# Performance work log

Hardware: AMD Instinct MI355X
Metric: run time of the kernel (lower is better)

The kernel has to match this reference:

```python
import jax, jax.numpy as jnp
import numpy as np

M_BITS = 8   # mantissa bits (m in BlockQuantize)
E_BITS = 8   # exponent bits (e)
GROUP_D = 64 # column-group width from group_shapes [64,64]


def bfp_quantize_2d(W, d=GROUP_D, m=M_BITS, e=E_BITS):
    """Faithful vectorized BlockQuantize2D with calculate_bias=True.
    Groups = 64-wide column blocks spanning all rows (tensor.reshape(-1,d)[start::new_width])."""
    a, b = W.shape
    nw = b // d
    # [nw, a*d]: each row is one quantization group
    blocks = W.reshape(a, nw, d).transpose(1, 0, 2).reshape(nw, a * d)
    maxv = jnp.max(jnp.abs(blocks), axis=1, keepdims=True)
    bias = 2.0 ** e - jnp.log2(maxv) + jnp.log2(2.0 - 2.0 ** (-m + 1)) - 1.0
    max_exp = 2.0 ** e - 1.0 - bias
    max_val = 2.0 ** max_exp * (1.0 + (1.0 - 2.0 ** (-m - 1)))
    sign = jnp.sign(blocks)
    absx = jnp.clip(jnp.abs(blocks), -max_val, max_val)  # lower bound negative -> no-op, as in source
    exponent = jnp.floor(jnp.log2(absx + 1e-40))
    mantissa = absx / 2.0 ** exponent                    # in [1, 2)
    group_exp = jnp.max(exponent, axis=1, keepdims=True)
    group_exp = jnp.where(group_exp + bias < 1.0, -bias, group_exp)
    # shiftTruncateInBinaryForm
    factor = 2 ** (m - 1)                                # 128
    sm = (mantissa * factor).astype(jnp.int32)           # [128, 256)
    shift = jnp.clip((group_exp - exponent).astype(jnp.int32), 0, 31)
    shifted = jnp.right_shift(sm, shift)
    safe = jnp.maximum(shifted, 1)
    bitlen = (jnp.floor(jnp.log2(safe.astype(jnp.float32))) + 1.0).astype(jnp.int32)
    mask = jnp.where(bitlen > 8, jnp.left_shift(jnp.int32(255), bitlen - 8), jnp.int32(255))
    trunc = jnp.bitwise_and(shifted, mask).astype(jnp.float32) / factor
    q = sign * trunc * 2.0 ** group_exp
    return q.reshape(nw, a, d).transpose(1, 0, 2).reshape(a, b)


def apply_rope(t, cos, sin):
    """t: [b,s,h,hd]; complex rotation on (even, odd) pairs as in apply_rotary_emb."""
    tr = t.reshape(*t.shape[:-1], -1, 2)
    te, to = tr[..., 0], tr[..., 1]
    c = cos[None, :, None, :]
    s = sin[None, :, None, :]
    oe = te * c - to * s
    oo = te * s + to * c
    return jnp.stack([oe, oo], axis=-1).reshape(t.shape)


def setup_inputs() -> dict:
    key = jax.random.key(0)
    k = jax.random.split(key, 5)
    dim, n_heads, n_kv, hd = 4096, 32, 8, 128
    b, s = 1, 2048
    x = jax.random.normal(k[0], (b, s, dim), jnp.float32)
    wq = jax.random.normal(k[1], (n_heads * hd, dim), jnp.float32) * 0.02
    wk = jax.random.normal(k[2], (n_kv * hd, dim), jnp.float32) * 0.02
    wv = jax.random.normal(k[3], (n_kv * hd, dim), jnp.float32) * 0.02
    wo = jax.random.normal(k[4], (dim, n_heads * hd), jnp.float32) * 0.02
    inv_freq = 1.0 / (10000.0 ** (jnp.arange(0, hd, 2, dtype=jnp.float32) / hd))
    ang = jnp.outer(jnp.arange(s, dtype=jnp.float32), inv_freq)  # [s, hd/2]
    return {"x": x, "wq": wq, "wk": wk, "wv": wv, "wo": wo,
            "freqs_cos": jnp.cos(ang), "freqs_sin": jnp.sin(ang)}


def reference(x, wq, wk, wv, wo, freqs_cos, freqs_sin):
    b, s, dim = x.shape
    n_heads, n_kv, hd = 32, 8, 128
    n_rep = n_heads // n_kv
    # block-floating-point quantization of projection weights (per-64-column groups)
    wq_q = bfp_quantize_2d(wq)
    wk_q = bfp_quantize_2d(wk)
    wv_q = bfp_quantize_2d(wv)
    wo_q = bfp_quantize_2d(wo)
    q = jnp.einsum('bsd,od->bso', x, wq_q).reshape(b, s, n_heads, hd)
    kk = jnp.einsum('bsd,od->bso', x, wk_q).reshape(b, s, n_kv, hd)
    v = jnp.einsum('bsd,od->bso', x, wv_q).reshape(b, s, n_kv, hd)
    q = apply_rope(q, freqs_cos, freqs_sin)
    kk = apply_rope(kk, freqs_cos, freqs_sin)
    # repeat_kv: GQA expand kv heads by n_rep
    kk = jnp.repeat(kk, n_rep, axis=2)  # [b,s,n_heads,hd]
    v = jnp.repeat(v, n_rep, axis=2)
    scores = jnp.einsum('bshd,bthd->bhst', q, kk) / jnp.sqrt(jnp.float32(hd))
    causal = jnp.triu(jnp.full((s, s), -jnp.inf, dtype=scores.dtype), k=1)
    probs = jax.nn.softmax(scores + causal, axis=-1)
    out = jnp.einsum('bhst,bthd->bshd', probs, v).reshape(b, s, n_heads * hd)
    return jnp.einsum('bso,do->bsd', out, wo_q)
```

## Files before the change

kernel.cpp:

```cpp
#include <hip/hip_runtime.h>
#include <hip/hip_bf16.h>

typedef __hip_bfloat16 hbf16;
typedef __bf16 bf16x8 __attribute__((ext_vector_type(8)));
typedef float f32x4 __attribute__((ext_vector_type(4)));

#define MFMA16(a, b, c) __builtin_amdgcn_mfma_f32_16x16x32_bf16((a), (b), (c), 0, 0, 0)

#define ASYNC16(ldsaddr, gaddr)                                                        \
  __builtin_amdgcn_global_load_lds(                                                    \
      (__attribute__((address_space(1))) void*)(void*)(gaddr),                         \
      (__attribute__((address_space(3))) void*)(ldsaddr), 16, 0, 0)

static __device__ __forceinline__ float fexp2(float x) {
#if __has_builtin(__builtin_amdgcn_exp2f)
  return __builtin_amdgcn_exp2f(x);
#else
  return exp2f(x);
#endif
}

__global__ void quant_max_kernel(const float* __restrict__ wq, const float* __restrict__ wk,
                                 const float* __restrict__ wv, const float* __restrict__ wo,
                                 unsigned int* __restrict__ gmaxs) {
  const int my = blockIdx.y;
  const float* W;
  int slotBase, rowsPerSplit;
  if (my == 0) { W = wq; slotBase = 0;   rowsPerSplit = 512; }
  else if (my == 1) { W = wk; slotBase = 64;  rowsPerSplit = 128; }
  else if (my == 2) { W = wv; slotBase = 128; rowsPerSplit = 128; }
  else { W = wo; slotBase = 192; rowsPerSplit = 512; }
  const int tid = threadIdx.x;
  const int group = blockIdx.x & 63;
  const int split = blockIdx.x >> 6;
  const int c4 = (tid & 15) * 4;
  const int rs = tid >> 4;
  const float* base = W + (size_t)(split * rowsPerSplit) * 4096 + group * 64 + c4;
  float m = 0.f;
  for (int r = rs; r < rowsPerSplit; r += 16) {
    float4 v = *(const float4*)(base + (size_t)r * 4096);
    m = fmaxf(m, fmaxf(fmaxf(fabsf(v.x), fabsf(v.y)), fmaxf(fabsf(v.z), fabsf(v.w))));
  }
  for (int d = 1; d < 64; d <<= 1) m = fmaxf(m, __shfl_xor(m, d, 64));
  __shared__ float wm_[4];
  if ((tid & 63) == 0) wm_[tid >> 6] = m;
  __syncthreads();
  if (tid == 0) {
    m = fmaxf(fmaxf(wm_[0], wm_[1]), fmaxf(wm_[2], wm_[3]));
    gmaxs[(slotBase + group) * 8 + split] = __float_as_uint(m);
  }
}

__device__ __forceinline__ void quant_body(const float* __restrict__ W, hbf16* __restrict__ Wq,
                                           const unsigned int* __restrict__ gmaxs, int slotBase,
                                           int n4, int block0, int nblocks) {
  const int stride = nblocks * 256;
  const int idx0 = block0 * 256 + (int)threadIdx.x;
  if (idx0 >= n4) return;
  const int slot = slotBase + ((idx0 & 1023) >> 4);
  unsigned int mb = 0;
#pragma unroll
  for (int sp = 0; sp < 8; ++sp) mb = max(mb, gmaxs[slot * 8 + sp]);
  int gex = (int)((mb >> 23) & 255) - 127;
  float s = __uint_as_float((unsigned)(134 - gex) << 23);
  float inv = __uint_as_float((unsigned)(120 + gex) << 23);
  for (int idx = idx0; idx < n4; idx += stride) {
    float4 w = *(const float4*)(W + (size_t)idx * 4);
    hbf16 t[4];
    t[0] = __float2bfloat16(truncf(w.x * s) * inv);
    t[1] = __float2bfloat16(truncf(w.y * s) * inv);
    t[2] = __float2bfloat16(truncf(w.z * s) * inv);
    t[3] = __float2bfloat16(truncf(w.w * s) * inv);
    *(uint2*)(Wq + (size_t)idx * 4) = *(uint2*)t;
  }
}

__global__ void prep_kernel(const float* __restrict__ wq, const float* __restrict__ wk,
                            const float* __restrict__ wv, const float* __restrict__ x,
                            hbf16* __restrict__ Wqkv, hbf16* __restrict__ xb,
                            const unsigned int* __restrict__ gmaxs) {
  const int my = blockIdx.y;
  if (my == 0) {
    quant_body(wq, Wqkv, gmaxs, 0, 4096 * 4096 / 4, blockIdx.x, gridDim.x);
  } else if (my == 1) {
    quant_body(wk, Wqkv + (size_t)4096 * 4096, gmaxs, 64, 1024 * 4096 / 4, blockIdx.x, gridDim.x);
  } else if (my == 2) {
    quant_body(wv, Wqkv + (size_t)5120 * 4096, gmaxs, 128, 1024 * 4096 / 4, blockIdx.x, gridDim.x);
  } else {
    const int stride = gridDim.x * 256;
    for (int idx = blockIdx.x * 256 + threadIdx.x; idx < 2048 * 4096 / 4; idx += stride) {
      float4 v = *(const float4*)(x + (size_t)idx * 4);
      hbf16 t[4] = {__float2bfloat16(v.x), __float2bfloat16(v.y),
                    __float2bfloat16(v.z), __float2bfloat16(v.w)};
      *(uint2*)(xb + (size_t)idx * 4) = *(uint2*)t;
    }
  }
}

__global__ void postproc_kernel(const float* __restrict__ wo, hbf16* __restrict__ woq,
                                const unsigned int* __restrict__ gmaxs,
                                const float* __restrict__ qkv, const float* __restrict__ Cs,
                                const float* __restrict__ Sn, hbf16* __restrict__ qrope,
                                hbf16* __restrict__ krope, hbf16* __restrict__ Vt, float qscale) {
  __shared__ float tile[64][65];
  const int bid = blockIdx.x;
  const int tid = threadIdx.x;
  if (bid < 2048) {
    quant_body(wo, woq, gmaxs, 192, 4096 * 4096 / 4, bid, 2048);
  } else if (bid < 18432) {
    int i = (bid - 2048) * 256 + tid;
    int s = i >> 11, p = i & 2047, t = p & 63;
    float2 q = *(const float2*)(qkv + (size_t)s * 6144 + p * 2);
    float c = Cs[s * 64 + t] * qscale, sn = Sn[s * 64 + t] * qscale;
    hbf16 o[2] = {__float2bfloat16(q.x * c - q.y * sn), __float2bfloat16(q.x * sn + q.y * c)};
    *(unsigned int*)(qrope + (size_t)s * 4096 + p * 2) = *(unsigned int*)o;
  } else if (bid < 22528) {
    int i = (bid - 18432) * 256 + tid;
    int s = i >> 9, p = i & 511, t = p & 63;
    float2 q = *(const float2*)(qkv + (size_t)s * 6144 + 4096 + p * 2);
    float c = Cs[s * 64 + t], sn = Sn[s * 64 + t];
    hbf16 o[2] = {__float2bfloat16(q.x * c - q.y * sn), __float2bfloat16(q.x * sn + q.y * c)};
    *(unsigned int*)(krope + (size_t)s * 1024 + p * 2) = *(unsigned int*)o;
  } else {
    int id = bid - 22528;
    int g = id & 7, sb = (id >> 3) & 31, db = id >> 8;
    int c = tid & 63;
    for (int r = tid >> 6; r < 64; r += 4)
      tile[r][c] = qkv[(size_t)(sb * 64 + r) * 6144 + 5120 + g * 128 + db * 64 + c];
    __syncthreads();
    for (int r = tid >> 6; r < 64; r += 4)
      Vt[(size_t)g * 262144 + (size_t)(db * 64 + r) * 2048 + sb * 64 + c] =
          __float2bfloat16(tile[c][r]);
  }
}

template <int BN>
__global__ __launch_bounds__(256) void gemm_bt_kernel(const hbf16* __restrict__ A,
                                                      const hbf16* __restrict__ Bt,
                                                      float* __restrict__ C, int N) {
  constexpr int K = 4096;
  constexpr int NF = BN / 32;
  __shared__ __align__(16) hbf16 sA[128 * 64];
  __shared__ __align__(16) hbf16 sB[BN * 64];
  const int tid = threadIdx.x;
  const int wave = tid >> 6, lane = tid & 63;
  const int l15 = lane & 15, quad = lane >> 4;
  const int bm = blockIdx.x, bn = blockIdx.y;
  const int wm = (wave >> 1) * 64, wn = (wave & 1) * (BN / 2);

  const char* Ab = (const char*)(A + (size_t)bm * 128 * K);
  const char* Bb = (const char*)(Bt + (size_t)bn * BN * K);
  char* sAb = (char*)sA;
  char* sBb = (char*)sB;

  f32x4 acc[4][NF];
#pragma unroll
  for (int i = 0; i < 4; ++i)
#pragma unroll
    for (int n = 0; n < NF; ++n) acc[i][n] = (f32x4){0.f, 0.f, 0.f, 0.f};

  for (int kk = 0; kk < K; kk += 64) {
#pragma unroll
    for (int r = 0; r < 4; ++r) {
      int f = r * 4096 + tid * 16;
      int row = f >> 7;
      int lc = ((f >> 4) & 7) ^ (row & 7);
      ASYNC16(sAb + f, Ab + (size_t)row * (K * 2) + kk * 2 + lc * 16);
    }
#pragma unroll
    for (int r = 0; r < NF; ++r) {
      int f = r * 4096 + tid * 16;
      int row = f >> 7;
      int lc = ((f >> 4) & 7) ^ (row & 7);
      ASYNC16(sBb + f, Bb + (size_t)row * (K * 2) + kk * 2 + lc * 16);
    }
    __syncthreads();
#pragma unroll
    for (int kc = 0; kc < 2; ++kc) {
      bf16x8 af[4], bg[NF];
#pragma unroll
      for (int i = 0; i < 4; ++i)
        af[i] = *(const bf16x8*)(sAb + (wm + i * 16 + l15) * 128 +
                                 (((kc << 2) | quad) ^ (l15 & 7)) * 16);
#pragma unroll
      for (int n = 0; n < NF; ++n)
        bg[n] = *(const bf16x8*)(sBb + (wn + n * 16 + l15) * 128 +
                                 (((kc << 2) | quad) ^ (l15 & 7)) * 16);
#pragma unroll
      for (int i = 0; i < 4; ++i)
#pragma unroll
        for (int n = 0; n < NF; ++n) acc[i][n] = MFMA16(af[i], bg[n], acc[i][n]);
    }
    __syncthreads();
  }
#pragma unroll
  for (int i = 0; i < 4; ++i) {
    int row = bm * 128 + wm + i * 16 + quad * 4;
#pragma unroll
    for (int n = 0; n < NF; ++n) {
      float* cp = C + (size_t)row * N + bn * BN + wn + n * 16 + l15;
#pragma unroll
      for (int r = 0; r < 4; ++r) cp[(size_t)r * N] = acc[i][n][r];
    }
  }
}

__global__ __launch_bounds__(256, 4) void attn_kernel(const hbf16* __restrict__ Q,
                                                      const hbf16* __restrict__ Kr,
                                                      const hbf16* __restrict__ Vt,
                                                      hbf16* __restrict__ O) {
  __shared__ __align__(16) hbf16 sK[64 * 128];
  __shared__ __align__(16) hbf16 sV[128 * 64];
  const int tid = threadIdx.x;
  const int wave = tid >> 6, lane = tid & 63;
  const int l15 = lane & 15, quad = lane >> 4;
  const int bid = blockIdx.x;
  const int h = bid >> 5;
  const int qb = (31 - (bid & 31) + 8 * ((bid >> 8) & 3)) & 31;
  const int g = h >> 2;
  const int qrow0 = qb * 64 + wave * 16;
  const int qrow = qrow0 + l15;

  bf16x8 qf[4];
  {
    const hbf16* qp = Q + (size_t)qrow * 4096 + h * 128 + quad * 8;
#pragma unroll
    for (int kc = 0; kc < 4; ++kc) qf[kc] = *(const bf16x8*)(qp + kc * 32);
  }
  f32x4 of[8];
#pragma unroll
  for (int nf = 0; nf < 8; ++nf) of[nf] = (f32x4){0.f, 0.f, 0.f, 0.f};
  float m_i = -1e30f, l_i = 0.f;

  const char* Kb = (const char*)Kr + (size_t)g * 256;
  const char* Vb = (const char*)Vt + (size_t)g * 524288;
  char* sKb = (char*)sK;
  char* sVb = (char*)sV;

  const int nkb = qb + 1;
  for (int kb = 0; kb < nkb; ++kb) {
#pragma unroll
    for (int r = 0; r < 4; ++r) {
      int f = r * 4096 + tid * 16;
      {
        int row = f >> 8;
        int lc = ((f >> 4) & 15) ^ (row & 15);
        ASYNC16(sKb + f, Kb + (size_t)(kb * 64 + row) * 2048 + lc * 16);
      }
      {
        int row = f >> 7;
        int lc = ((f >> 4) & 7) ^ (row & 7);
        ASYNC16(sVb + f, Vb + (size_t)row * 4096 + kb * 128 + lc * 16);
      }
    }
    __syncthreads();

    f32x4 sacc[4];
#pragma unroll
    for (int n = 0; n < 4; ++n) sacc[n] = (f32x4){0.f, 0.f, 0.f, 0.f};
#pragma unroll
    for (int n = 0; n < 4; ++n)
#pragma unroll
      for (int kc = 0; kc < 4; ++kc) {
        bf16x8 kf = *(const bf16x8*)(sKb + (n * 16 + l15) * 256 +
                                     (((kc << 2) | quad) ^ l15) * 16);
        sacc[n] = MFMA16(kf, qf[kc], sacc[n]);
      }

    float p[4][4];
    float mx = -1e30f;
    if (kb == qb) {
      const int key0 = kb * 64 + quad * 4;
#pragma unroll
      for (int n = 0; n < 4; ++n)
#pragma unroll
        for (int r = 0; r < 4; ++r) {
          float s = sacc[n][r];
          s = (key0 + n * 16 + r > qrow) ? -1e30f : s;
          p[n][r] = s;
          mx = fmaxf(mx, s);
        }
    } else {
#pragma unroll
      for (int n = 0; n < 4; ++n)
#pragma unroll
        for (int r = 0; r < 4; ++r) {
          p[n][r] = sacc[n][r];
          mx = fmaxf(mx, sacc[n][r]);
        }
    }
    mx = fmaxf(mx, __shfl_xor(mx, 16, 64));
    mx = fmaxf(mx, __shfl_xor(mx, 32, 64));
    float mnew = fmaxf(m_i, mx);
    float alpha = fexp2(m_i - mnew);
    m_i = mnew;
    float sum = 0.f;
#pragma unroll
    for (int n = 0; n < 4; ++n)
#pragma unroll
      for (int r = 0; r < 4; ++r) {
        p[n][r] = fexp2(p[n][r] - mnew);
        sum += p[n][r];
      }
    sum += __shfl_xor(sum, 16, 64);
    sum += __shfl_xor(sum, 32, 64);
    l_i = l_i * alpha + sum;
#pragma unroll
    for (int nf = 0; nf < 8; ++nf)
#pragma unroll
      for (int r = 0; r < 4; ++r) of[nf][r] *= alpha;

    unsigned pk[8];
#pragma unroll
    for (int n = 0; n < 4; ++n)
#pragma unroll
      for (int h2 = 0; h2 < 2; ++h2) {
        hbf16 t2[2] = {__float2bfloat16(p[n][2 * h2]), __float2bfloat16(p[n][2 * h2 + 1])};
        pk[n * 2 + h2] = *(unsigned*)t2;
      }

    const int sa = ((quad & 1) << 5) + l15;
    const int sb2 = sa + 16;
#pragma unroll
    for (int kc = 0; kc < 2; ++kc) {
      unsigned a0 = __shfl((int)pk[kc * 4 + 0], sa, 64);
      unsigned a1 = __shfl((int)pk[kc * 4 + 1], sa, 64);
      unsigned a2 = __shfl((int)pk[kc * 4 + 2], sa, 64);
      unsigned a3 = __shfl((int)pk[kc * 4 + 3], sa, 64);
      unsigned b0 = __shfl((int)pk[kc * 4 + 0], sb2, 64);
      unsigned b1 = __shfl((int)pk[kc * 4 + 1], sb2, 64);
      unsigned b2 = __shfl((int)pk[kc * 4 + 2], sb2, 64);
      unsigned b3 = __shfl((int)pk[kc * 4 + 3], sb2, 64);
      union {
        unsigned u[4];
        bf16x8 v;
      } pf;
      pf.u[0] = (quad < 2) ? a0 : a2;
      pf.u[1] = (quad < 2) ? a1 : a3;
      pf.u[2] = (quad < 2) ? b0 : b2;
      pf.u[3] = (quad < 2) ? b1 : b3;
#pragma unroll
      for (int nf = 0; nf < 8; ++nf) {
        bf16x8 vf = *(const bf16x8*)(sVb + (nf * 16 + l15) * 128 +
                                     (((kc << 2) | quad) ^ (l15 & 7)) * 16);
        of[nf] = MFMA16(vf, pf.v, of[nf]);
      }
    }
    __syncthreads();
  }

  const float invl = 1.f / l_i;
#pragma unroll
  for (int nf = 0; nf < 8; ++nf) {
    hbf16 t4[4];
#pragma unroll
    for (int r = 0; r < 4; ++r) t4[r] = __float2bfloat16(of[nf][r] * invl);
    *(uint2*)(O + (size_t)qrow * 4096 + h * 128 + nf * 16 + quad * 4) = *(uint2*)t4;
  }
}

extern "C" void kernel_launch(void* const* d_in, const int* in_sizes, int n_in,
                              void* d_out, int out_size, void* d_ws, size_t ws_size,
                              hipStream_t stream) {
  const float* x = (const float*)d_in[0];
  const float* wq = (const float*)d_in[1];
  const float* wk = (const float*)d_in[2];
  const float* wv = (const float*)d_in[3];
  const float* wo = (const float*)d_in[4];
  const float* fc = (const float*)d_in[5];
  const float* fs = (const float*)d_in[6];
  float* out = (float*)d_out;

  char* w = (char*)d_ws;
  size_t off = 0;
  auto alloc = [&](size_t bytes) -> char* {
    char* p = w + off;
    off += (bytes + 255) & ~(size_t)255;
    return p;
  };
  unsigned int* gmaxs = (unsigned int*)alloc(256 * 8 * 4);
  hbf16* xb = (hbf16*)alloc((size_t)2048 * 4096 * 2);
  hbf16* wqkv = (hbf16*)alloc((size_t)6144 * 4096 * 2);
  float* qkv = (float*)alloc((size_t)2048 * 6144 * 4);
  hbf16* qrope = (hbf16*)alloc((size_t)2048 * 4096 * 2);
  hbf16* krope = (hbf16*)alloc((size_t)2048 * 1024 * 2);
  hbf16* vt = (hbf16*)alloc((size_t)8 * 128 * 2048 * 2);
  hbf16* woq = wqkv;
  hbf16* attno = (hbf16*)qkv;

  const float kSc = 0.12753139668280277f;

  quant_max_kernel<<<dim3(512, 4), 256, 0, stream>>>(wq, wk, wv, wo, gmaxs);
  prep_kernel<<<dim3(2048, 4), 256, 0, stream>>>(wq, wk, wv, x, wqkv, xb, gmaxs);
  gemm_bt_kernel<96><<<dim3(16, 64), 256, 0, stream>>>(xb, wqkv, qkv, 6144);
  postproc_kernel<<<23040, 256, 0, stream>>>(wo, woq, gmaxs, qkv, fc, fs, qrope, krope, vt, kSc);
  attn_kernel<<<1024, 256, 0, stream>>>(qrope, krope, vt, attno);
  gemm_bt_kernel<64><<<dim3(16, 64), 256, 0, stream>>>(attno, woq, out, 4096);
  (void)in_sizes; (void)n_in; (void)out_size; (void)ws_size;
}
```

Before: 573.5 us.

## Replace GEMM with 8-wave 128x256 tile kernel using triple-buffered async LDS pipeline

```diff
diff --git a/kernel.cpp b/kernel.cpp
--- a/kernel.cpp
+++ b/kernel.cpp
@@ -134,71 +134,116 @@
   }
 }
 
-template <int BN>
-__global__ __launch_bounds__(256) void gemm_bt_kernel(const hbf16* __restrict__ A,
-                                                      const hbf16* __restrict__ Bt,
-                                                      float* __restrict__ C, int N) {
+__global__ __launch_bounds__(512, 2) void gemm8_kernel(const hbf16* __restrict__ A,
+                                                       const hbf16* __restrict__ Bt,
+                                                       float* __restrict__ C, int N) {
   constexpr int K = 4096;
-  constexpr int NF = BN / 32;
-  __shared__ __align__(16) hbf16 sA[128 * 64];
-  __shared__ __align__(16) hbf16 sB[BN * 64];
+  constexpr int NT = K / 64;
+  constexpr int TILE = 128 * 128 + 256 * 128;
+  __shared__ __align__(16) char smem[3 * TILE];
   const int tid = threadIdx.x;
   const int wave = tid >> 6, lane = tid & 63;
   const int l15 = lane & 15, quad = lane >> 4;
   const int bm = blockIdx.x, bn = blockIdx.y;
-  const int wm = (wave >> 1) * 64, wn = (wave & 1) * (BN / 2);
+  const int wm = (wave >> 2) * 64, wn = (wave & 3) * 64;
 
   const char* Ab = (const char*)(A + (size_t)bm * 128 * K);
-  const char* Bb = (const char*)(Bt + (size_t)bn * BN * K);
-  char* sAb = (char*)sA;
-  char* sBb = (char*)sB;
-
-  f32x4 acc[4][NF];
+  const char* Bb = (const char*)(Bt + (size_t)bn * 256 * K);
+
+  f32x4 acc[4][4];
 #pragma unroll
   for (int i = 0; i < 4; ++i)
 #pragma unroll
-    for (int n = 0; n < NF; ++n) acc[i][n] = (f32x4){0.f, 0.f, 0.f, 0.f};
-
-  for (int kk = 0; kk < K; kk += 64) {
-#pragma unroll
-    for (int r = 0; r < 4; ++r) {
-      int f = r * 4096 + tid * 16;
+    for (int n = 0; n < 4; ++n) acc[i][n] = (f32x4){0.f, 0.f, 0.f, 0.f};
+
+  auto stageA = [&](char* buf, int kk) {
+#pragma unroll
+    for (int r = 0; r < 2; ++r) {
+      int f = r * 8192 + tid * 16;
       int row = f >> 7;
       int lc = ((f >> 4) & 7) ^ (row & 7);
-      ASYNC16(sAb + f, Ab + (size_t)row * (K * 2) + kk * 2 + lc * 16);
-    }
-#pragma unroll
-    for (int r = 0; r < NF; ++r) {
-      int f = r * 4096 + tid * 16;
+      ASYNC16(buf + f, Ab + (size_t)row * (K * 2) + kk * 2 + lc * 16);
+    }
+  };
+  auto stageB = [&](char* buf, int kk) {
+#pragma unroll
+    for (int r = 0; r < 4; ++r) {
+      int f = r * 8192 + tid * 16;
       int row = f >> 7;
       int lc = ((f >> 4) & 7) ^ (row & 7);
-      ASYNC16(sBb + f, Bb + (size_t)row * (K * 2) + kk * 2 + lc * 16);
-    }
-    __syncthreads();
+      ASYNC16(buf + 16384 + f, Bb + (size_t)row * (K * 2) + kk * 2 + lc * 16);
+    }
+  };
+
+  stageA(smem, 0);
+  stageB(smem, 0);
+  stageA(smem + TILE, 64);
+  stageB(smem + TILE, 64);
+  asm volatile("s_waitcnt vmcnt(6)" ::: "memory");
+  __builtin_amdgcn_s_barrier();
+
+  int cur = 0;
+  for (int t = 0; t < NT; ++t) {
+    const char* sa = smem + cur * TILE;
+    const char* sb = sa + 16384;
+    const int nxt2 = (cur >= 1) ? cur - 1 : 2;
+    char* stg = smem + nxt2 * TILE;
+    const int kk2 = ((t + 2 < NT) ? t + 2 : NT - 1) * 64;
+
+    bf16x8 af[2][4], b0[2][2];
 #pragma unroll
     for (int kc = 0; kc < 2; ++kc) {
-      bf16x8 af[4], bg[NF];
+      const int cx = (((kc << 2) | quad) ^ (l15 & 7)) * 16;
 #pragma unroll
       for (int i = 0; i < 4; ++i)
-        af[i] = *(const bf16x8*)(sAb + (wm + i * 16 + l15) * 128 +
-                                 (((kc << 2) | quad) ^ (l15 & 7)) * 16);
-#pragma unroll
-      for (int n = 0; n < NF; ++n)
-        bg[n] = *(const bf16x8*)(sBb + (wn + n * 16 + l15) * 128 +
-                                 (((kc << 2) | quad) ^ (l15 & 7)) * 16);
+        af[kc][i] = *(const bf16x8*)(sa + (wm + i * 16 + l15) * 128 + cx);
+#pragma unroll
+      for (int n = 0; n < 2; ++n)
+        b0[kc][n] = *(const bf16x8*)(sb + (wn + n * 16 + l15) * 128 + cx);
+    }
+    stageA(stg, kk2);
+    __builtin_amdgcn_s_barrier();
+    __builtin_amdgcn_s_setprio(1);
+#pragma unroll
+    for (int kc = 0; kc < 2; ++kc)
 #pragma unroll
       for (int i = 0; i < 4; ++i)
 #pragma unroll
-        for (int n = 0; n < NF; ++n) acc[i][n] = MFMA16(af[i], bg[n], acc[i][n]);
-    }
-    __syncthreads();
-  }
+        for (int n = 0; n < 2; ++n) acc[i][n] = MFMA16(af[kc][i], b0[kc][n], acc[i][n]);
+    __builtin_amdgcn_s_setprio(0);
+    __builtin_amdgcn_s_barrier();
+
+    bf16x8 b1[2][2];
+#pragma unroll
+    for (int kc = 0; kc < 2; ++kc) {
+      const int cx = (((kc << 2) | quad) ^ (l15 & 7)) * 16;
+#pragma unroll
+      for (int n = 0; n < 2; ++n)
+        b1[kc][n] = *(const bf16x8*)(sb + (wn + (n + 2) * 16 + l15) * 128 + cx);
+    }
+    stageB(stg, kk2);
+    asm volatile("s_waitcnt vmcnt(6)" ::: "memory");
+    __builtin_amdgcn_s_barrier();
+    __builtin_amdgcn_s_setprio(1);
+#pragma unroll
+    for (int kc = 0; kc < 2; ++kc)
+#pragma unroll
+      for (int i = 0; i < 4; ++i)
+#pragma unroll
+        for (int n = 0; n < 2; ++n)
+          acc[i][n + 2] = MFMA16(af[kc][i], b1[kc][n], acc[i][n + 2]);
+    __builtin_amdgcn_s_setprio(0);
+    __builtin_amdgcn_s_barrier();
+
+    cur = (cur == 2) ? 0 : cur + 1;
+  }
+
 #pragma unroll
   for (int i = 0; i < 4; ++i) {
     int row = bm * 128 + wm + i * 16 + quad * 4;
 #pragma unroll
-    for (int n = 0; n < NF; ++n) {
-      float* cp = C + (size_t)row * N + bn * BN + wn + n * 16 + l15;
+    for (int n = 0; n < 4; ++n) {
+      float* cp = C + (size_t)row * N + bn * 256 + wn + n * 16 + l15;
 #pragma unroll
       for (int r = 0; r < 4; ++r) cp[(size_t)r * N] = acc[i][n][r];
     }
@@ -392,9 +437,9 @@
 
   quant_max_kernel<<<dim3(512, 4), 256, 0, stream>>>(wq, wk, wv, wo, gmaxs);
   prep_kernel<<<dim3(2048, 4), 256, 0, stream>>>(wq, wk, wv, x, wqkv, xb, gmaxs);
-  gemm_bt_kernel<96><<<dim3(16, 64), 256, 0, stream>>>(xb, wqkv, qkv, 6144);
+  gemm8_kernel<<<dim3(16, 24), 512, 0, stream>>>(xb, wqkv, qkv, 6144);
   postproc_kernel<<<23040, 256, 0, stream>>>(wo, woq, gmaxs, qkv, fc, fs, qrope, krope, vt, kSc);
   attn_kernel<<<1024, 256, 0, stream>>>(qrope, krope, vt, attno);
-  gemm_bt_kernel<64><<<dim3(16, 64), 256, 0, stream>>>(attno, woq, out, 4096);
+  gemm8_kernel<<<dim3(16, 16), 512, 0, stream>>>(attno, woq, out, 4096);
   (void)in_sizes; (void)n_in; (void)out_size; (void)ws_size;
 }
```

Measured after the change: 555.7 us. -3.1%, faster.
